# Kernel optimization log

Hardware: AMD Instinct MI355X
Metric: run time of the kernel (lower is better)

The kernel has to match this reference:

```python
import jax, jax.numpy as jnp
import numpy as np

N = 100000   # nodes
E = 1600000  # edges
IN = 128     # in_dim
H = 64       # hidden_dim
EPS = 1e-5


def layer_norm(x, g, b):
    mu = x.mean(-1, keepdims=True)
    v = ((x - mu) ** 2).mean(-1, keepdims=True)
    return (x - mu) * jax.lax.rsqrt(v + EPS) * g + b


def gcn_conv(x, W, b, src, dst, dinv):
    # PyG GCNConv: x' = D^{-1/2}(A+I)D^{-1/2} X W + b (degrees include self-loops)
    h = x @ W                                   # [N, H]
    coef = dinv[src] * dinv[dst]                # [E]
    agg = jax.ops.segment_sum(h[src] * coef[:, None], dst, num_segments=N)
    agg = agg + h * (dinv * dinv)[:, None]      # self-loop term
    return agg + b


def setup_inputs() -> dict:
    key = jax.random.key(0)
    ks = jax.random.split(key, 12)
    inp = {
        "x": jax.random.normal(ks[0], (N, IN), jnp.float32),
        "edge_index": jax.random.randint(ks[1], (2, E), 0, N, dtype=jnp.int64
                                         if jax.config.jax_enable_x64 else jnp.int32),
    }
    dims = [(IN, H), (H, H), (H, H)]
    for i, (di, do) in enumerate(dims, start=1):
        inp[f"W{i}"] = jax.random.normal(ks[2 * i], (di, do), jnp.float32) / np.sqrt(di)
        inp[f"b{i}"] = jnp.zeros((do,), jnp.float32)
        inp[f"g{i}"] = jnp.ones((do,), jnp.float32)
        inp[f"be{i}"] = jnp.zeros((do,), jnp.float32)
    inp["Wh"] = jax.random.normal(ks[11], (H, 1), jnp.float32) / np.sqrt(H)
    inp["bh"] = jnp.zeros((1,), jnp.float32)
    return inp


def reference(x, edge_index, W1, b1, g1, be1, W2, b2, g2, be2, W3, b3, g3, be3, Wh, bh):
    src, dst = edge_index[0], edge_index[1]
    deg = jax.ops.segment_sum(jnp.ones((E,), x.dtype), dst, num_segments=N) + 1.0
    dinv = jax.lax.rsqrt(deg)
    for W, b, g, be in ((W1, b1, g1, be1), (W2, b2, g2, be2), (W3, b3, g3, be3)):
        x = gcn_conv(x, W, b, src, dst, dinv)
        x = layer_norm(x, g, be)
        x = jax.nn.gelu(x, approximate=False)  # F.gelu default = exact erf
        # dropout omitted (eval mode / deterministic reference)
    return (x @ Wh + bh).squeeze(-1)  # [N]
```

## Files before the change

### kernel.cpp

```cpp
#include <hip/hip_runtime.h>
#include <math.h>

#define NODES 100000
#define EDGES 1600000
#define NBUCK 196
#define BCAP2 12288
#define EPB 4096

typedef __attribute__((ext_vector_type(8))) short short8;
typedef __attribute__((ext_vector_type(4))) float floatx4;
typedef __attribute__((ext_vector_type(4))) unsigned uv4;

__device__ __forceinline__ float gsum8(float x) {
#pragma unroll
  for (int o = 4; o > 0; o >>= 1) x += __shfl_xor(x, o, 64);
  return x;
}

__device__ __forceinline__ short f2bf(float f) {
  union { float f; unsigned u; } v;
  v.f = f;
  unsigned r = 0x7fffu + ((v.u >> 16) & 1u);
  return (short)((v.u + r) >> 16);
}
__device__ __forceinline__ float bflo(unsigned p) {
  union { unsigned u; float f; } v; v.u = p << 16; return v.f;
}
__device__ __forceinline__ float bfhi(unsigned p) {
  union { unsigned u; float f; } v; v.u = p & 0xffff0000u; return v.f;
}

__global__ __launch_bounds__(256) void k_bin2(const int* __restrict__ src,
                                              const int* __restrict__ dst,
                                              int* __restrict__ bins,
                                              int* __restrict__ gcur) {
  __shared__ int cnt[NBUCK], gbase[NBUCK], lcur[NBUCK];
  int t = threadIdx.x;
  for (int i = t; i < NBUCK; i += 256) cnt[i] = 0;
  __syncthreads();
  int base = blockIdx.x * EPB;
  int s[16], d[16];
#pragma unroll
  for (int j = 0; j < 16; ++j) {
    int e = base + j * 256 + t;
    if (e < EDGES) {
      s[j] = src[e];
      d[j] = dst[e];
      atomicAdd(&cnt[d[j] >> 9], 1);
    } else {
      d[j] = -1;
    }
  }
  __syncthreads();
  for (int i = t; i < NBUCK; i += 256) {
    int c = cnt[i];
    gbase[i] = c ? atomicAdd(&gcur[i], c) : 0;
    lcur[i] = 0;
  }
  __syncthreads();
#pragma unroll
  for (int j = 0; j < 16; ++j) {
    if (d[j] >= 0) {
      int bk = d[j] >> 9;
      int lp = atomicAdd(&lcur[bk], 1);
      int pos = gbase[bk] + lp;
      if (pos < BCAP2) bins[bk * BCAP2 + pos] = s[j] | ((d[j] & 511) << 17);
    }
  }
}

__global__ void k_scanb(const int* __restrict__ gcur, int* __restrict__ bbase,
                        int* __restrict__ rowptr) {
  __shared__ int sm[256];
  int t = threadIdx.x;
  int v = 0;
  if (t < NBUCK) { v = gcur[t]; if (v > BCAP2) v = BCAP2; }
  sm[t] = v;
  __syncthreads();
  for (int o = 1; o < 256; o <<= 1) {
    int u = (t >= o) ? sm[t - o] : 0;
    __syncthreads();
    sm[t] += u;
    __syncthreads();
  }
  if (t < NBUCK) bbase[t] = sm[t] - v;
  if (t == NBUCK - 1) {
    bbase[NBUCK] = sm[t];
    rowptr[NODES] = sm[t];
  }
}

__global__ __launch_bounds__(256) void k_fillb2(const int* __restrict__ bins,
                                                const int* __restrict__ gcur,
                                                const int* __restrict__ bbase,
                                                int* __restrict__ rowptr,
                                                float* __restrict__ dinv,
                                                int* __restrict__ csr) {
  __shared__ int cnt[512], cur[512], wtot[4];
  int b = blockIdx.x, t = threadIdx.x;
  cnt[t] = 0; cnt[t + 256] = 0;
  __syncthreads();
  int c = gcur[b]; if (c > BCAP2) c = BCAP2;
  const int* bp = &bins[(size_t)b * BCAP2];
  for (int i = t; i < c; i += 256)
    atomicAdd(&cnt[(bp[i] >> 17) & 511], 1);
  __syncthreads();
  int a0 = cnt[2 * t], a1 = cnt[2 * t + 1];
  int s = a0 + a1;
  int lane = t & 63, w = t >> 6;
  int inc = s;
#pragma unroll
  for (int o = 1; o < 64; o <<= 1) {
    int u = __shfl_up(inc, o, 64);
    if (lane >= o) inc += u;
  }
  if (lane == 63) wtot[w] = inc;
  __syncthreads();
  int wpre = 0;
  for (int ww = 0; ww < w; ++ww) wpre += wtot[ww];
  int base = bbase[b];
  int r0 = base + wpre + inc - s;
  int r1 = r0 + a0;
  int n0 = b * 512 + 2 * t, n1 = n0 + 1;
  if (n0 < NODES) { rowptr[n0] = r0; dinv[n0] = rsqrtf((float)a0 + 1.0f); }
  if (n1 < NODES) { rowptr[n1] = r1; dinv[n1] = rsqrtf((float)a1 + 1.0f); }
  cur[2 * t] = r0; cur[2 * t + 1] = r1;
  __syncthreads();
  for (int i = t; i < c; i += 256) {
    int pk = bp[i];
    int p = atomicAdd(&cur[(pk >> 17) & 511], 1);
    csr[p] = pk & 0x1FFFF;
  }
}

template <int K>
__global__ __launch_bounds__(256) void k_gemm_f32(const float* __restrict__ x,
                                                  const float* __restrict__ W,
                                                  const float* __restrict__ dinv,
                                                  short* __restrict__ hs) {
  constexpr int KP = K + 8;
  __shared__ short wt[64 * KP];
  for (int idx = threadIdx.x; idx < K * 64; idx += 256) {
    int k = idx >> 6, n = idx & 63;
    wt[n * KP + k] = f2bf(W[idx]);
  }
  __syncthreads();
  int wid = threadIdx.x >> 6, lane = threadIdx.x & 63;
  int tile = blockIdx.x * 4 + wid;
  if (tile * 16 >= NODES) return;
  int m = lane & 15, q = lane >> 4;

  short8 bfr[4][K / 32];
#pragma unroll
  for (int ct = 0; ct < 4; ++ct)
#pragma unroll
    for (int ks = 0; ks < K / 32; ++ks)
      bfr[ct][ks] = *reinterpret_cast<const short8*>(&wt[(ct * 16 + m) * KP + ks * 32 + q * 8]);

  floatx4 acc[4];
#pragma unroll
  for (int ct = 0; ct < 4; ++ct) acc[ct] = {0.f, 0.f, 0.f, 0.f};
  int r0 = tile * 16;
#pragma unroll
  for (int ks = 0; ks < K / 32; ++ks) {
    const float* xp = &x[(size_t)(r0 + m) * K + ks * 32 + q * 8];
    floatx4 a0 = *reinterpret_cast<const floatx4*>(xp);
    floatx4 a1 = *reinterpret_cast<const floatx4*>(xp + 4);
    short8 af;
#pragma unroll
    for (int j = 0; j < 4; ++j) { af[j] = f2bf(a0[j]); af[4 + j] = f2bf(a1[j]); }
#pragma unroll
    for (int ct = 0; ct < 4; ++ct)
      acc[ct] = __builtin_amdgcn_mfma_f32_16x16x32_bf16(af, bfr[ct][ks], acc[ct], 0, 0, 0);
  }
  float dv[4];
#pragma unroll
  for (int r = 0; r < 4; ++r) dv[r] = dinv[r0 + q * 4 + r];
#pragma unroll
  for (int ct = 0; ct < 4; ++ct)
#pragma unroll
    for (int r = 0; r < 4; ++r) {
      int row = r0 + q * 4 + r, col = ct * 16 + m;
      hs[row * 64 + col] = f2bf(acc[ct][r] * dv[r]);
    }
}

__global__ __launch_bounds__(256) void k_gemm_bf(const short* __restrict__ x,
                                                 const float* __restrict__ W,
                                                 const float* __restrict__ dinv,
                                                 short* __restrict__ hs) {
  constexpr int K = 64, KP = K + 8;
  __shared__ short wt[64 * KP];
  for (int idx = threadIdx.x; idx < K * 64; idx += 256) {
    int k = idx >> 6, n = idx & 63;
    wt[n * KP + k] = f2bf(W[idx]);
  }
  __syncthreads();
  int wid = threadIdx.x >> 6, lane = threadIdx.x & 63;
  int tile = blockIdx.x * 4 + wid;
  if (tile * 16 >= NODES) return;
  int m = lane & 15, q = lane >> 4;

  short8 bfr[4][2];
#pragma unroll
  for (int ct = 0; ct < 4; ++ct)
#pragma unroll
    for (int ks = 0; ks < 2; ++ks)
      bfr[ct][ks] = *reinterpret_cast<const short8*>(&wt[(ct * 16 + m) * KP + ks * 32 + q * 8]);

  floatx4 acc[4];
#pragma unroll
  for (int ct = 0; ct < 4; ++ct) acc[ct] = {0.f, 0.f, 0.f, 0.f};
  int r0 = tile * 16;
#pragma unroll
  for (int ks = 0; ks < 2; ++ks) {
    short8 af = *reinterpret_cast<const short8*>(&x[(size_t)(r0 + m) * K + ks * 32 + q * 8]);
#pragma unroll
    for (int ct = 0; ct < 4; ++ct)
      acc[ct] = __builtin_amdgcn_mfma_f32_16x16x32_bf16(af, bfr[ct][ks], acc[ct], 0, 0, 0);
  }
  float dv[4];
#pragma unroll
  for (int r = 0; r < 4; ++r) dv[r] = dinv[r0 + q * 4 + r];
#pragma unroll
  for (int ct = 0; ct < 4; ++ct)
#pragma unroll
    for (int r = 0; r < 4; ++r) {
      int row = r0 + q * 4 + r, col = ct * 16 + m;
      hs[row * 64 + col] = f2bf(acc[ct][r] * dv[r]);
    }
}

template <int FINAL>
__global__ __launch_bounds__(256) void k_agg(const short* __restrict__ hs,
                                             const float* __restrict__ dinv,
                                             const int* __restrict__ rowptr,
                                             const int* __restrict__ csr,
                                             const float* __restrict__ bias,
                                             const float* __restrict__ gam,
                                             const float* __restrict__ bet,
                                             const float* __restrict__ Wh,
                                             const float* __restrict__ bh,
                                             void* __restrict__ out) {
  const uv4* hsv = (const uv4*)hs;
  int lane = threadIdx.x & 63, wid = threadIdx.x >> 6;
  int g = lane >> 3, q = lane & 7;
  int n = blockIdx.x * 32 + wid * 8 + g;
  int e0 = rowptr[n], e1 = rowptr[n + 1];
  float dn = dinv[n];
  uv4 sv = hsv[(size_t)n * 8 + q];
  float acc[8];
#pragma unroll
  for (int w = 0; w < 4; ++w) { acc[2 * w] = bflo(sv[w]); acc[2 * w + 1] = bfhi(sv[w]); }

  int srcb = lane & 0x38;
  for (int base = e0; base < e1; base += 8) {
    int cnt = e1 - base;
    if (cnt > 8) cnt = 8;
    int a = base + (q < cnt ? q : 0);
    int sidx = csr[a];
    int s[8];
#pragma unroll
    for (int j = 0; j < 8; ++j) s[j] = __shfl(sidx, srcb | j, 64);
    uv4 v[8];
#pragma unroll
    for (int j = 0; j < 8; ++j) v[j] = hsv[(size_t)s[j] * 8 + q];
    if (cnt == 8) {
#pragma unroll
      for (int j = 0; j < 8; ++j)
#pragma unroll
        for (int w = 0; w < 4; ++w) { acc[2 * w] += bflo(v[j][w]); acc[2 * w + 1] += bfhi(v[j][w]); }
    } else {
#pragma unroll
      for (int j = 0; j < 8; ++j)
        if (j < cnt)
#pragma unroll
          for (int w = 0; w < 4; ++w) { acc[2 * w] += bflo(v[j][w]); acc[2 * w + 1] += bfhi(v[j][w]); }
    }
  }

  const floatx4* bi4 = (const floatx4*)bias;
  floatx4 b0 = bi4[q * 2], b1 = bi4[q * 2 + 1];
#pragma unroll
  for (int f = 0; f < 4; ++f) { acc[f] = acc[f] * dn + b0[f]; acc[f + 4] = acc[f + 4] * dn + b1[f]; }

  float lsum = 0.f;
#pragma unroll
  for (int f = 0; f < 8; ++f) lsum += acc[f];
  float mu = gsum8(lsum) * (1.0f / 64.0f);
  float d[8], lvar = 0.f;
#pragma unroll
  for (int f = 0; f < 8; ++f) { d[f] = acc[f] - mu; lvar += d[f] * d[f]; }
  float rs = rsqrtf(gsum8(lvar) * (1.0f / 64.0f) + 1e-5f);
  const floatx4* gm4 = (const floatx4*)gam;
  const floatx4* bt4 = (const floatx4*)bet;
  floatx4 g0 = gm4[q * 2], g1 = gm4[q * 2 + 1];
  floatx4 t0 = bt4[q * 2], t1 = bt4[q * 2 + 1];
  float u[8];
#pragma unroll
  for (int f = 0; f < 8; ++f) {
    float gv = (f < 4) ? g0[f] : g1[f - 4];
    float tv = (f < 4) ? t0[f] : t1[f - 4];
    float vv = d[f] * rs * gv + tv;
    u[f] = 0.5f * vv * (1.0f + erff(vv * 0.70710678118654752f));
  }
  if (FINAL) {
    const floatx4* wh4 = (const floatx4*)Wh;
    floatx4 w0 = wh4[q * 2], w1 = wh4[q * 2 + 1];
    float lp = 0.f;
#pragma unroll
    for (int f = 0; f < 4; ++f) lp += u[f] * w0[f] + u[f + 4] * w1[f];
    float p = gsum8(lp);
    if (q == 0) ((float*)out)[n] = p + bh[0];
  } else {
    uv4 pk;
#pragma unroll
    for (int w = 0; w < 4; ++w)
      pk[w] = (unsigned)(unsigned short)f2bf(u[2 * w]) |
              ((unsigned)(unsigned short)f2bf(u[2 * w + 1]) << 16);
    ((uv4*)out)[(size_t)n * 8 + q] = pk;
  }
}

extern "C" void kernel_launch(void* const* d_in, const int* in_sizes, int n_in,
                              void* d_out, int out_size, void* d_ws, size_t ws_size,
                              hipStream_t stream) {
  const float* x  = (const float*)d_in[0];
  const int* ei   = (const int*)d_in[1];
  const float* W1 = (const float*)d_in[2];
  const float* b1 = (const float*)d_in[3];
  const float* g1 = (const float*)d_in[4];
  const float* be1= (const float*)d_in[5];
  const float* W2 = (const float*)d_in[6];
  const float* b2 = (const float*)d_in[7];
  const float* g2 = (const float*)d_in[8];
  const float* be2= (const float*)d_in[9];
  const float* W3 = (const float*)d_in[10];
  const float* b3 = (const float*)d_in[11];
  const float* g3 = (const float*)d_in[12];
  const float* be3= (const float*)d_in[13];
  const float* Wh = (const float*)d_in[14];
  const float* bh = (const float*)d_in[15];
  const int* srcp = ei;
  const int* dstp = ei + EDGES;

  char* ws = (char*)d_ws;
  size_t off = 0;
  auto take = [&](size_t bytes) {
    char* p = ws + off;
    off = (off + bytes + 255) & ~(size_t)255;
    return p;
  };
  float* dinv = (float*)take((size_t)NODES * 4);
  int* rowptr = (int*)take((size_t)(NODES + 1) * 4);
  int* bbase  = (int*)take((size_t)(NBUCK + 1) * 4);
  int* csr    = (int*)take((size_t)EDGES * 4);
  short* hs   = (short*)take((size_t)NODES * 64 * 2);
  short* xb   = (short*)take((size_t)NODES * 64 * 2);
  int* bins   = (int*)hs;
  int* gcur   = (int*)xb;

  (void)hipMemsetAsync(gcur, 0, (size_t)NBUCK * 4, stream);
  k_bin2<<<(EDGES + EPB - 1) / EPB, 256, 0, stream>>>(srcp, dstp, bins, gcur);
  k_scanb<<<1, 256, 0, stream>>>(gcur, bbase, rowptr);
  k_fillb2<<<NBUCK, 256, 0, stream>>>(bins, gcur, bbase, rowptr, dinv, csr);

  int gemm_grid = (NODES / 16 + 3) / 4;
  k_gemm_f32<128><<<gemm_grid, 256, 0, stream>>>(x, W1, dinv, hs);
  k_agg<0><<<NODES / 32, 256, 0, stream>>>(hs, dinv, rowptr, csr, b1, g1, be1, nullptr, nullptr, xb);
  k_gemm_bf<<<gemm_grid, 256, 0, stream>>>(xb, W2, dinv, hs);
  k_agg<0><<<NODES / 32, 256, 0, stream>>>(hs, dinv, rowptr, csr, b2, g2, be2, nullptr, nullptr, xb);
  k_gemm_bf<<<gemm_grid, 256, 0, stream>>>(xb, W3, dinv, hs);
  k_agg<1><<<NODES / 32, 256, 0, stream>>>(hs, dinv, rowptr, csr, b3, g3, be3, Wh, bh, d_out);
}
```

Before: 292.8 us.

## Fuse next-layer GEMM into aggregation kernel and fold bucket scan into fill

The layer-2 and layer-3 dense transforms move into the aggregation kernel. Each block aggregates 32 nodes, applies LayerNorm and GELU, stages the dinv-scaled bf16 result in LDS, and multiplies it by the next weight matrix with MFMA before writing hs. This removes two GEMM launches and the round trip of the intermediate activations through global memory. The single-block bucket scan kernel is also merged into the fill kernel, where every block redundantly recomputes the 196-entry prefix sum. In exchange, each aggregation block now converts the full 64x64 weight matrix to bf16 and adds a barrier.

```diff
diff --git a/kernel.cpp b/kernel.cpp
--- a/kernel.cpp
+++ b/kernel.cpp
@@ -69,40 +69,30 @@
   }
 }
 
-__global__ void k_scanb(const int* __restrict__ gcur, int* __restrict__ bbase,
-                        int* __restrict__ rowptr) {
-  __shared__ int sm[256];
-  int t = threadIdx.x;
-  int v = 0;
-  if (t < NBUCK) { v = gcur[t]; if (v > BCAP2) v = BCAP2; }
-  sm[t] = v;
-  __syncthreads();
-  for (int o = 1; o < 256; o <<= 1) {
-    int u = (t >= o) ? sm[t - o] : 0;
-    __syncthreads();
-    sm[t] += u;
-    __syncthreads();
-  }
-  if (t < NBUCK) bbase[t] = sm[t] - v;
-  if (t == NBUCK - 1) {
-    bbase[NBUCK] = sm[t];
-    rowptr[NODES] = sm[t];
-  }
-}
-
 __global__ __launch_bounds__(256) void k_fillb2(const int* __restrict__ bins,
                                                 const int* __restrict__ gcur,
-                                                const int* __restrict__ bbase,
                                                 int* __restrict__ rowptr,
                                                 float* __restrict__ dinv,
                                                 int* __restrict__ csr) {
+  __shared__ int bsm[256];
   __shared__ int cnt[512], cur[512], wtot[4];
   int b = blockIdx.x, t = threadIdx.x;
+  int v = 0;
+  if (t < NBUCK) { v = gcur[t]; if (v > BCAP2) v = BCAP2; }
+  bsm[t] = v;
   cnt[t] = 0; cnt[t + 256] = 0;
   __syncthreads();
-  int c = gcur[b]; if (c > BCAP2) c = BCAP2;
+  for (int o = 1; o < 256; o <<= 1) {
+    int u = (t >= o) ? bsm[t - o] : 0;
+    __syncthreads();
+    bsm[t] += u;
+    __syncthreads();
+  }
+  if (b == 0 && t == NBUCK - 1) rowptr[NODES] = bsm[t];
+  int cb = gcur[b]; if (cb > BCAP2) cb = BCAP2;
+  int base = bsm[b] - cb;
   const int* bp = &bins[(size_t)b * BCAP2];
-  for (int i = t; i < c; i += 256)
+  for (int i = t; i < cb; i += 256)
     atomicAdd(&cnt[(bp[i] >> 17) & 511], 1);
   __syncthreads();
   int a0 = cnt[2 * t], a1 = cnt[2 * t + 1];
@@ -118,7 +108,6 @@
   __syncthreads();
   int wpre = 0;
   for (int ww = 0; ww < w; ++ww) wpre += wtot[ww];
-  int base = bbase[b];
   int r0 = base + wpre + inc - s;
   int r1 = r0 + a0;
   int n0 = b * 512 + 2 * t, n1 = n0 + 1;
@@ -126,7 +115,7 @@
   if (n1 < NODES) { rowptr[n1] = r1; dinv[n1] = rsqrtf((float)a1 + 1.0f); }
   cur[2 * t] = r0; cur[2 * t + 1] = r1;
   __syncthreads();
-  for (int i = t; i < c; i += 256) {
+  for (int i = t; i < cb; i += 256) {
     int pk = bp[i];
     int p = atomicAdd(&cur[(pk >> 17) & 511], 1);
     csr[p] = pk & 0x1FFFF;
@@ -139,7 +128,7 @@
                                                   const float* __restrict__ dinv,
                                                   short* __restrict__ hs) {
   constexpr int KP = K + 8;
-  __shared__ short wt[64 * KP];
+  __shared__ __align__(16) short wt[64 * KP];
   for (int idx = threadIdx.x; idx < K * 64; idx += 256) {
     int k = idx >> 6, n = idx & 63;
     wt[n * KP + k] = f2bf(W[idx]);
@@ -185,63 +174,127 @@
     }
 }
 
-__global__ __launch_bounds__(256) void k_gemm_bf(const short* __restrict__ x,
-                                                 const float* __restrict__ W,
+__global__ __launch_bounds__(256) void k_aggg(const short* __restrict__ hs,
+                                              const float* __restrict__ dinv,
+                                              const int* __restrict__ rowptr,
+                                              const int* __restrict__ csr,
+                                              const float* __restrict__ bias,
+                                              const float* __restrict__ gam,
+                                              const float* __restrict__ bet,
+                                              const float* __restrict__ W,
+                                              short* __restrict__ hsn) {
+  __shared__ __align__(16) short wt[64 * 72];
+  __shared__ __align__(16) short ut[32 * 72];
+  int t = threadIdx.x;
+  for (int idx = t; idx < 4096; idx += 256) {
+    int k = idx >> 6, n = idx & 63;
+    wt[n * 72 + k] = f2bf(W[idx]);
+  }
+  const uv4* hsv = (const uv4*)hs;
+  int lane = t & 63, wid = t >> 6;
+  int g = lane >> 3, q = lane & 7;
+  int nb0 = blockIdx.x * 32;
+  int r = wid * 8 + g;
+  int n = nb0 + r;
+  int e0 = rowptr[n], e1 = rowptr[n + 1];
+  float dn = dinv[n];
+  uv4 sv = hsv[(size_t)n * 8 + q];
+  float acc[8];
+#pragma unroll
+  for (int w = 0; w < 4; ++w) { acc[2 * w] = bflo(sv[w]); acc[2 * w + 1] = bfhi(sv[w]); }
+
+  int srcb = lane & 0x38;
+  for (int base = e0; base < e1; base += 8) {
+    int cnt = e1 - base;
+    if (cnt > 8) cnt = 8;
+    int a = base + (q < cnt ? q : 0);
+    int sidx = csr[a];
+    int s[8];
+#pragma unroll
+    for (int j = 0; j < 8; ++j) s[j] = __shfl(sidx, srcb | j, 64);
+    uv4 v[8];
+#pragma unroll
+    for (int j = 0; j < 8; ++j) v[j] = hsv[(size_t)s[j] * 8 + q];
+    if (cnt == 8) {
+#pragma unroll
+      for (int j = 0; j < 8; ++j)
+#pragma unroll
+        for (int w = 0; w < 4; ++w) { acc[2 * w] += bflo(v[j][w]); acc[2 * w + 1] += bfhi(v[j][w]); }
+    } else {
+#pragma unroll
+      for (int j = 0; j < 8; ++j)
+        if (j < cnt)
+#pragma unroll
+          for (int w = 0; w < 4; ++w) { acc[2 * w] += bflo(v[j][w]); acc[2 * w + 1] += bfhi(v[j][w]); }
+    }
+  }
+
+  const floatx4* bi4 = (const floatx4*)bias;
+  floatx4 b0 = bi4[q * 2], b1 = bi4[q * 2 + 1];
+#pragma unroll
+  for (int f = 0; f < 4; ++f) { acc[f] = acc[f] * dn + b0[f]; acc[f + 4] = acc[f + 4] * dn + b1[f]; }
+
+  float lsum = 0.f;
+#pragma unroll
+  for (int f = 0; f < 8; ++f) lsum += acc[f];
+  float mu = gsum8(lsum) * (1.0f / 64.0f);
+  float d[8], lvar = 0.f;
+#pragma unroll
+  for (int f = 0; f < 8; ++f) { d[f] = acc[f] - mu; lvar += d[f] * d[f]; }
+  float rs = rsqrtf(gsum8(lvar) * (1.0f / 64.0f) + 1e-5f);
+  const floatx4* gm4 = (const floatx4*)gam;
+  const floatx4* bt4 = (const floatx4*)bet;
+  floatx4 g0 = gm4[q * 2], g1 = gm4[q * 2 + 1];
+  floatx4 t0 = bt4[q * 2], t1 = bt4[q * 2 + 1];
+  short8 us;
+#pragma unroll
+  for (int f = 0; f < 8; ++f) {
+    float gv = (f < 4) ? g0[f] : g1[f - 4];
+    float tv = (f < 4) ? t0[f] : t1[f - 4];
+    float vv = d[f] * rs * gv + tv;
+    float u = 0.5f * vv * (1.0f + erff(vv * 0.70710678118654752f));
+    us[f] = f2bf(u * dn);
+  }
+  *reinterpret_cast<short8*>(&ut[r * 72 + q * 8]) = us;
+  __syncthreads();
+
+  int m = lane & 15, q2 = lane >> 4;
+  int tile = wid >> 1, cb = (wid & 1) * 2;
+  short8 bfr[2][2];
+#pragma unroll
+  for (int ct = 0; ct < 2; ++ct)
+#pragma unroll
+    for (int ks = 0; ks < 2; ++ks)
+      bfr[ct][ks] = *reinterpret_cast<const short8*>(&wt[((cb + ct) * 16 + m) * 72 + ks * 32 + q2 * 8]);
+  floatx4 ac[2];
+#pragma unroll
+  for (int ct = 0; ct < 2; ++ct) ac[ct] = {0.f, 0.f, 0.f, 0.f};
+#pragma unroll
+  for (int ks = 0; ks < 2; ++ks) {
+    short8 af = *reinterpret_cast<const short8*>(&ut[(tile * 16 + m) * 72 + ks * 32 + q2 * 8]);
+#pragma unroll
+    for (int ct = 0; ct < 2; ++ct)
+      ac[ct] = __builtin_amdgcn_mfma_f32_16x16x32_bf16(af, bfr[ct][ks], ac[ct], 0, 0, 0);
+  }
+#pragma unroll
+  for (int ct = 0; ct < 2; ++ct)
+#pragma unroll
+    for (int rr = 0; rr < 4; ++rr) {
+      int row = nb0 + tile * 16 + q2 * 4 + rr, col = (cb + ct) * 16 + m;
+      hsn[row * 64 + col] = f2bf(ac[ct][rr]);
+    }
+}
+
+__global__ __launch_bounds__(256) void k_agg_fin(const short* __restrict__ hs,
                                                  const float* __restrict__ dinv,
-                                                 short* __restrict__ hs) {
-  constexpr int K = 64, KP = K + 8;
-  __shared__ short wt[64 * KP];
-  for (int idx = threadIdx.x; idx < K * 64; idx += 256) {
-    int k = idx >> 6, n = idx & 63;
-    wt[n * KP + k] = f2bf(W[idx]);
-  }
-  __syncthreads();
-  int wid = threadIdx.x >> 6, lane = threadIdx.x & 63;
-  int tile = blockIdx.x * 4 + wid;
-  if (tile * 16 >= NODES) return;
-  int m = lane & 15, q = lane >> 4;
-
-  short8 bfr[4][2];
-#pragma unroll
-  for (int ct = 0; ct < 4; ++ct)
-#pragma unroll
-    for (int ks = 0; ks < 2; ++ks)
-      bfr[ct][ks] = *reinterpret_cast<const short8*>(&wt[(ct * 16 + m) * KP + ks * 32 + q * 8]);
-
-  floatx4 acc[4];
-#pragma unroll
-  for (int ct = 0; ct < 4; ++ct) acc[ct] = {0.f, 0.f, 0.f, 0.f};
-  int r0 = tile * 16;
-#pragma unroll
-  for (int ks = 0; ks < 2; ++ks) {
-    short8 af = *reinterpret_cast<const short8*>(&x[(size_t)(r0 + m) * K + ks * 32 + q * 8]);
-#pragma unroll
-    for (int ct = 0; ct < 4; ++ct)
-      acc[ct] = __builtin_amdgcn_mfma_f32_16x16x32_bf16(af, bfr[ct][ks], acc[ct], 0, 0, 0);
-  }
-  float dv[4];
-#pragma unroll
-  for (int r = 0; r < 4; ++r) dv[r] = dinv[r0 + q * 4 + r];
-#pragma unroll
-  for (int ct = 0; ct < 4; ++ct)
-#pragma unroll
-    for (int r = 0; r < 4; ++r) {
-      int row = r0 + q * 4 + r, col = ct * 16 + m;
-      hs[row * 64 + col] = f2bf(acc[ct][r] * dv[r]);
-    }
-}
-
-template <int FINAL>
-__global__ __launch_bounds__(256) void k_agg(const short* __restrict__ hs,
-                                             const float* __restrict__ dinv,
-                                             const int* __restrict__ rowptr,
-                                             const int* __restrict__ csr,
-                                             const float* __restrict__ bias,
-                                             const float* __restrict__ gam,
-                                             const float* __restrict__ bet,
-                                             const float* __restrict__ Wh,
-                                             const float* __restrict__ bh,
-                                             void* __restrict__ out) {
+                                                 const int* __restrict__ rowptr,
+                                                 const int* __restrict__ csr,
+                                                 const float* __restrict__ bias,
+                                                 const float* __restrict__ gam,
+                                                 const float* __restrict__ bet,
+                                                 const float* __restrict__ Wh,
+                                                 const float* __restrict__ bh,
+                                                 float* __restrict__ out) {
   const uv4* hsv = (const uv4*)hs;
   int lane = threadIdx.x & 63, wid = threadIdx.x >> 6;
   int g = lane >> 3, q = lane & 7;
@@ -252,7 +305,6 @@
   float acc[8];
 #pragma unroll
   for (int w = 0; w < 4; ++w) { acc[2 * w] = bflo(sv[w]); acc[2 * w + 1] = bfhi(sv[w]); }
-
   int srcb = lane & 0x38;
   for (int base = e0; base < e1; base += 8) {
     int cnt = e1 - base;
@@ -278,12 +330,10 @@
           for (int w = 0; w < 4; ++w) { acc[2 * w] += bflo(v[j][w]); acc[2 * w + 1] += bfhi(v[j][w]); }
     }
   }
-
   const floatx4* bi4 = (const floatx4*)bias;
   floatx4 b0 = bi4[q * 2], b1 = bi4[q * 2 + 1];
 #pragma unroll
   for (int f = 0; f < 4; ++f) { acc[f] = acc[f] * dn + b0[f]; acc[f + 4] = acc[f + 4] * dn + b1[f]; }
-
   float lsum = 0.f;
 #pragma unroll
   for (int f = 0; f < 8; ++f) lsum += acc[f];
@@ -296,30 +346,20 @@
   const floatx4* bt4 = (const floatx4*)bet;
   floatx4 g0 = gm4[q * 2], g1 = gm4[q * 2 + 1];
   floatx4 t0 = bt4[q * 2], t1 = bt4[q * 2 + 1];
-  float u[8];
+  const floatx4* wh4 = (const floatx4*)Wh;
+  floatx4 w0 = wh4[q * 2], w1 = wh4[q * 2 + 1];
+  float lp = 0.f;
 #pragma unroll
   for (int f = 0; f < 8; ++f) {
     float gv = (f < 4) ? g0[f] : g1[f - 4];
     float tv = (f < 4) ? t0[f] : t1[f - 4];
+    float wv = (f < 4) ? w0[f] : w1[f - 4];
     float vv = d[f] * rs * gv + tv;
-    u[f] = 0.5f * vv * (1.0f + erff(vv * 0.70710678118654752f));
-  }
-  if (FINAL) {
-    const floatx4* wh4 = (const floatx4*)Wh;
-    floatx4 w0 = wh4[q * 2], w1 = wh4[q * 2 + 1];
-    float lp = 0.f;
-#pragma unroll
-    for (int f = 0; f < 4; ++f) lp += u[f] * w0[f] + u[f + 4] * w1[f];
-    float p = gsum8(lp);
-    if (q == 0) ((float*)out)[n] = p + bh[0];
-  } else {
-    uv4 pk;
-#pragma unroll
-    for (int w = 0; w < 4; ++w)
-      pk[w] = (unsigned)(unsigned short)f2bf(u[2 * w]) |
-              ((unsigned)(unsigned short)f2bf(u[2 * w + 1]) << 16);
-    ((uv4*)out)[(size_t)n * 8 + q] = pk;
-  }
+    float u = 0.5f * vv * (1.0f + erff(vv * 0.70710678118654752f));
+    lp += u * wv;
+  }
+  float p = gsum8(lp);
+  if (q == 0) out[n] = p + bh[0];
 }
 
 extern "C" void kernel_launch(void* const* d_in, const int* in_sizes, int n_in,
@@ -353,23 +393,19 @@
   };
   float* dinv = (float*)take((size_t)NODES * 4);
   int* rowptr = (int*)take((size_t)(NODES + 1) * 4);
-  int* bbase  = (int*)take((size_t)(NBUCK + 1) * 4);
   int* csr    = (int*)take((size_t)EDGES * 4);
-  short* hs   = (short*)take((size_t)NODES * 64 * 2);
-  short* xb   = (short*)take((size_t)NODES * 64 * 2);
-  int* bins   = (int*)hs;
-  int* gcur   = (int*)xb;
+  short* hs_a = (short*)take((size_t)NODES * 64 * 2);
+  short* hs_b = (short*)take((size_t)NODES * 64 * 2);
+  int* bins   = (int*)hs_a;
+  int* gcur   = (int*)hs_b;
 
   (void)hipMemsetAsync(gcur, 0, (size_t)NBUCK * 4, stream);
   k_bin2<<<(EDGES + EPB - 1) / EPB, 256, 0, stream>>>(srcp, dstp, bins, gcur);
-  k_scanb<<<1, 256, 0, stream>>>(gcur, bbase, rowptr);
-  k_fillb2<<<NBUCK, 256, 0, stream>>>(bins, gcur, bbase, rowptr, dinv, csr);
+  k_fillb2<<<NBUCK, 256, 0, stream>>>(bins, gcur, rowptr, dinv, csr);
 
   int gemm_grid = (NODES / 16 + 3) / 4;
-  k_gemm_f32<128><<<gemm_grid, 256, 0, stream>>>(x, W1, dinv, hs);
-  k_agg<0><<<NODES / 32, 256, 0, stream>>>(hs, dinv, rowptr, csr, b1, g1, be1, nullptr, nullptr, xb);
-  k_gemm_bf<<<gemm_grid, 256, 0, stream>>>(xb, W2, dinv, hs);
-  k_agg<0><<<NODES / 32, 256, 0, stream>>>(hs, dinv, rowptr, csr, b2, g2, be2, nullptr, nullptr, xb);
-  k_gemm_bf<<<gemm_grid, 256, 0, stream>>>(xb, W3, dinv, hs);
-  k_agg<1><<<NODES / 32, 256, 0, stream>>>(hs, dinv, rowptr, csr, b3, g3, be3, Wh, bh, d_out);
-}
+  k_gemm_f32<128><<<gemm_grid, 256, 0, stream>>>(x, W1, dinv, hs_a);
+  k_aggg<<<NODES / 32, 256, 0, stream>>>(hs_a, dinv, rowptr, csr, b1, g1, be1, W2, hs_b);
+  k_aggg<<<NODES / 32, 256, 0, stream>>>(hs_b, dinv, rowptr, csr, b2, g2, be2, W3, hs_a);
+  k_agg_fin<<<NODES / 32, 256, 0, stream>>>(hs_a, dinv, rowptr, csr, b3, g3, be3, Wh, bh, (float*)d_out);
+}
```

New measurement: 280.4 us. 4.3% less time.
